# Performance work log

Measured on AMD Instinct MI355X. Metric: run time of the kernel, lower is better.

The kernel has to match this reference:

```python
import jax, jax.numpy as jnp
import numpy as np

# LIF neuron constants (standard mem_update)
THRESH = 0.5
LENS = 0.5
DECAY = 0.25
EPS = 1e-5
NUM_HEADS = 8

@jax.custom_vjp
def act_fun(mem):
    return (mem > THRESH).astype(mem.dtype)

def _act_fwd(mem):
    return act_fun(mem), mem

def _act_bwd(mem, g):
    surrogate = (jnp.abs(mem - THRESH) < LENS).astype(g.dtype)
    return (g * surrogate,)

act_fun.defvjp(_act_fwd, _act_bwd)

def mem_update(x):
    # x: (T, ...) -> binary spikes (T, ...) via recurrent LIF dynamics
    def step(carry, xt):
        mem_old, spike = carry
        # spike is detached in the reset gate (torch .detach())
        mem = mem_old * DECAY * (1.0 - jax.lax.stop_gradient(spike)) + xt
        s = act_fun(mem)
        return (mem, s), s
    init = (jnp.zeros_like(x[0]), jnp.zeros_like(x[0]))
    _, out = jax.lax.scan(step, init, x)
    return out

def bn(x, gamma, beta, mean, var):
    # inference-mode BatchNorm1d over channel dim of (T,B,C,L)
    inv = gamma / jnp.sqrt(var + EPS)
    return x * inv[None, None, :, None] + (beta - mean * inv)[None, None, :, None]

def setup_inputs() -> dict:
    key = jax.random.key(0)
    ks = jax.random.split(key, 11)
    T, B, C, L = 4, 2, 384, 1024
    s = 1.0 / np.sqrt(C)
    return {
        "x": jax.random.normal(ks[0], (T, B, C, L), jnp.float32),
        "W_w": jax.random.normal(ks[1], (2 * C, C), jnp.float32) * s,
        "bn1_gamma": jax.random.uniform(ks[2], (2 * C,), jnp.float32, 0.5, 1.5),
        "bn1_beta": jax.random.normal(ks[3], (2 * C,), jnp.float32) * 0.1,
        "bn1_mean": jax.random.normal(ks[4], (2 * C,), jnp.float32) * 0.1,
        "bn1_var": jax.random.uniform(ks[5], (2 * C,), jnp.float32, 0.5, 1.5),
        "proj_w": jax.random.normal(ks[6], (C, C), jnp.float32) * s,
        "bn2_gamma": jax.random.uniform(ks[7], (C,), jnp.float32, 0.5, 1.5),
        "bn2_beta": jax.random.normal(ks[8], (C,), jnp.float32) * 0.1,
        "bn2_mean": jax.random.normal(ks[9], (C,), jnp.float32) * 0.1,
        "bn2_var": jax.random.uniform(ks[10], (C,), jnp.float32, 0.5, 1.5),
    }

def reference(x, W_w, bn1_gamma, bn1_beta, bn1_mean, bn1_var, proj_w, bn2_gamma, bn2_beta, bn2_mean, bn2_var):
    T, B, C, L = x.shape
    H = NUM_HEADS
    d = C // H
    x_feat = x
    xs = mem_update(x)                                   # binary spikes (T,B,C,L)
    y = jnp.einsum('oc,tbcl->tbol', W_w, xs)             # 1x1 conv C->2C
    y = bn(y, bn1_gamma, bn1_beta, bn1_mean, bn1_var)
    y = y.reshape(T, B, H, 2 * d, L)
    y1, y2 = y[:, :, :, :d, :], y[:, :, :, d:, :]
    xr = xs.reshape(T, B, H, d, L)
    attn = jnp.einsum('tbhdl,tbhdm->tbhlm', y1, xr)      # (L,L) per head
    attn = mem_update(attn)                              # binary spikes
    out = jnp.einsum('tbhdl,tbhlm->tbhdm', y2, attn)
    out = out.reshape(T, B, C, L)
    out = mem_update(out)
    out = jnp.einsum('oc,tbcl->tbol', proj_w, out)       # Wproj 1x1
    out = bn(out, bn2_gamma, bn2_beta, bn2_mean, bn2_var)
    return out + x_feat
```

## Files before the change

kernel.cpp:

```cpp
#include <hip/hip_runtime.h>

#define T_  4
#define B_  2
#define C_  384
#define L_  1024
#define H_  8
#define C2_ 768
#define S_  (B_*C_*L_)

typedef __attribute__((ext_vector_type(8))) short short8;
typedef __attribute__((ext_vector_type(4))) float floatx4;
typedef __attribute__((ext_vector_type(16))) float floatx16;

__device__ __forceinline__ unsigned bf16_rne(float v) {
    unsigned u = __float_as_uint(v);
    u += 0x7FFFu + ((u >> 16) & 1u);
    return u >> 16;
}
__device__ __forceinline__ float bf16_to_f(unsigned h) { return __uint_as_float(h << 16); }
__device__ __forceinline__ void split3(float v, unsigned& hi, unsigned& mi, unsigned& lo) {
    hi = bf16_rne(v);
    float r1 = v - bf16_to_f(hi);
    mi = bf16_rne(r1);
    float r2 = r1 - bf16_to_f(mi);
    lo = bf16_rne(r2);
}

__global__ __launch_bounds__(256) void scan_and_split(
    const float* __restrict__ src, unsigned short* __restrict__ dstT,
    unsigned short* __restrict__ xsF,
    const float* __restrict__ Wa, int n4a,
    unsigned short* __restrict__ hia, unsigned short* __restrict__ mia,
    unsigned short* __restrict__ loa,
    const float* __restrict__ Wb, int n4b,
    unsigned short* __restrict__ hib, unsigned short* __restrict__ mib,
    unsigned short* __restrict__ lob) {
    __shared__ unsigned short tile[64][72];
    const int tid = threadIdx.x;
    if (blockIdx.x >= 192) {
        int i = (blockIdx.x - 192) * 256 + tid;
        const float* W; unsigned short *hi, *mi, *lo;
        if (i < n4a) { W = Wa; hi = hia; mi = mia; lo = loa; }
        else {
            i -= n4a;
            if (i >= n4b) return;
            W = Wb; hi = hib; mi = mib; lo = lob;
        }
        float4 v = ((const float4*)W)[i];
        float vv[4] = {v.x, v.y, v.z, v.w};
        union { unsigned short us[4]; uint2 u2; } h, m, l;
#pragma unroll
        for (int e = 0; e < 4; e++) {
            unsigned hh, mm, ll; split3(vv[e], hh, mm, ll);
            h.us[e] = (unsigned short)hh; m.us[e] = (unsigned short)mm; l.us[e] = (unsigned short)ll;
        }
        ((uint2*)hi)[i] = h.u2; ((uint2*)mi)[i] = m.u2; ((uint2*)lo)[i] = l.u2;
        return;
    }
    const int job = blockIdx.x;
    const int l0 = (job & 15) * 64;
    const int c0 = ((job >> 4) % 6) * 64;
    const int b  = job / 96;
    const int row = tid >> 2, seg = tid & 3;
    float mem[16], sp[16];
#pragma unroll
    for (int e = 0; e < 16; e++) { mem[e] = 0.f; sp[e] = 0.f; }
    for (int t = 0; t < T_; t++) {
        const size_t base = ((size_t)((t*B_ + b)*C_ + c0 + row))*L_ + l0 + seg*16;
#pragma unroll
        for (int qq = 0; qq < 4; qq++) {
            float4 v = *(const float4*)(src + base + qq*4);
            float vv[4] = {v.x, v.y, v.z, v.w};
            unsigned bs[4];
#pragma unroll
            for (int s = 0; s < 4; s++) {
                int e = qq*4 + s;
                mem[e] = mem[e]*0.25f*(1.f - sp[e]) + vv[s];
                bool sb = mem[e] > 0.5f;
                sp[e] = sb ? 1.f : 0.f;
                bs[s] = sb ? 0x3F80u : 0u;
            }
            *(unsigned*)&tile[row][seg*16 + qq*4]     = bs[0] | (bs[1] << 16);
            *(unsigned*)&tile[row][seg*16 + qq*4 + 2] = bs[2] | (bs[3] << 16);
        }
        __syncthreads();
        {
            const int lr = tid >> 2, cs = tid & 3;
#pragma unroll
            for (int sub = 0; sub < 2; sub++) {
                unsigned wv[4];
#pragma unroll
                for (int p = 0; p < 4; p++) {
                    unsigned e0 = tile[cs*16 + sub*8 + p*2][lr];
                    unsigned e1 = tile[cs*16 + sub*8 + p*2 + 1][lr];
                    wv[p] = e0 | (e1 << 16);
                }
                uint4 o; o.x = wv[0]; o.y = wv[1]; o.z = wv[2]; o.w = wv[3];
                const int cc = c0 + cs*16 + sub*8;
                *(uint4*)(dstT + ((size_t)(t*B_ + b)*L_ + l0 + lr)*C_ + cc) = o;
                const int hh = cc / 48, kc = (cc % 48) >> 3;
                *(uint4*)(xsF + ((((size_t)(t*B_ + b)*H_ + hh)*6 + kc)*L_ + l0 + lr)*8) = o;
            }
        }
        __syncthreads();
    }
}

__global__ __launch_bounds__(256) void scan_transpose(const float* __restrict__ src,
                                                      unsigned short* __restrict__ dstT) {
    __shared__ unsigned short tile[64][72];
    const int tid = threadIdx.x;
    const int l0 = blockIdx.x * 64, c0 = blockIdx.y * 64, b = blockIdx.z;
    const int row = tid >> 2, seg = tid & 3;
    float mem[16], sp[16];
#pragma unroll
    for (int e = 0; e < 16; e++) { mem[e] = 0.f; sp[e] = 0.f; }
    for (int t = 0; t < T_; t++) {
        const size_t base = ((size_t)((t*B_ + b)*C_ + c0 + row))*L_ + l0 + seg*16;
#pragma unroll
        for (int qq = 0; qq < 4; qq++) {
            float4 v = *(const float4*)(src + base + qq*4);
            float vv[4] = {v.x, v.y, v.z, v.w};
            unsigned bs[4];
#pragma unroll
            for (int s = 0; s < 4; s++) {
                int e = qq*4 + s;
                mem[e] = mem[e]*0.25f*(1.f - sp[e]) + vv[s];
                bool sb = mem[e] > 0.5f;
                sp[e] = sb ? 1.f : 0.f;
                bs[s] = sb ? 0x3F80u : 0u;
            }
            *(unsigned*)&tile[row][seg*16 + qq*4]     = bs[0] | (bs[1] << 16);
            *(unsigned*)&tile[row][seg*16 + qq*4 + 2] = bs[2] | (bs[3] << 16);
        }
        __syncthreads();
        {
            const int lr = tid >> 2, cs = tid & 3;
#pragma unroll
            for (int sub = 0; sub < 2; sub++) {
                unsigned wv[4];
#pragma unroll
                for (int p = 0; p < 4; p++) {
                    unsigned e0 = tile[cs*16 + sub*8 + p*2][lr];
                    unsigned e1 = tile[cs*16 + sub*8 + p*2 + 1][lr];
                    wv[p] = e0 | (e1 << 16);
                }
                uint4 o; o.x = wv[0]; o.y = wv[1]; o.z = wv[2]; o.w = wv[3];
                *(uint4*)(dstT + ((size_t)(t*B_ + b)*L_ + l0 + lr)*C_ + c0 + cs*16 + sub*8) = o;
            }
        }
        __syncthreads();
    }
}

__global__ __launch_bounds__(256) void gemm1_mfma(
    const unsigned short* __restrict__ whi, const unsigned short* __restrict__ wmi,
    const unsigned short* __restrict__ wlo, const unsigned short* __restrict__ xsT,
    const float* __restrict__ g, const float* __restrict__ be,
    const float* __restrict__ mn, const float* __restrict__ vr,
    unsigned short* __restrict__ y1hi, unsigned short* __restrict__ y1mi,
    unsigned short* __restrict__ y1lo,
    unsigned short* __restrict__ y2hi, unsigned short* __restrict__ y2mi,
    unsigned short* __restrict__ y2lo) {
    __shared__ unsigned short smem[14080];
    const int tid = threadIdx.x;
    const int flat = blockIdx.x;
    const int tb = flat & 7;
    const int ii = flat >> 3;
    const int mt = ii >> 4, lt = ii & 15;
    const int l0 = lt * 64;
    const int w = tid >> 6, lane = tid & 63;
    const int q = lane >> 4, n15 = lane & 15;
    const int mw = (w & 1) * 48, lw = (w >> 1) * 32;

    floatx4 acc[3][2];
#pragma unroll
    for (int i = 0; i < 3; i++)
#pragma unroll
        for (int j = 0; j < 2; j++) acc[i][j] = (floatx4){0.f,0.f,0.f,0.f};

    for (int ck = 0; ck < C_; ck += 32) {
#pragma unroll
        for (int p = 0; p < 3; p++) {
            const unsigned short* wp = p == 0 ? whi : p == 1 ? wmi : wlo;
            unsigned short* ap = smem + p*3840;
            for (int s = tid; s < 384; s += 256) {
                int r = s >> 2, c = s & 3;
                *(uint4*)&ap[r*40 + c*8] = *(const uint4*)(wp + (size_t)(mt*96 + r)*C_ + ck + c*8);
            }
        }
        {
            int r = tid >> 2, c = tid & 3;
            *(uint4*)&smem[11520 + r*40 + c*8] =
                *(const uint4*)(xsT + ((size_t)tb*L_ + l0 + r)*C_ + ck + c*8);
        }
        __syncthreads();
        short8 bb[2];
#pragma unroll
        for (int in = 0; in < 2; in++)
            bb[in] = *(short8*)&smem[11520 + (lw + in*16 + n15)*40 + q*8];
#pragma unroll
        for (int im = 0; im < 3; im++) {
            short8 ah = *(short8*)&smem[       (mw + im*16 + n15)*40 + q*8];
            short8 am = *(short8*)&smem[3840 + (mw + im*16 + n15)*40 + q*8];
            short8 al = *(short8*)&smem[7680 + (mw + im*16 + n15)*40 + q*8];
#pragma unroll
            for (int in = 0; in < 2; in++) {
                acc[im][in] = __builtin_amdgcn_mfma_f32_16x16x32_bf16(ah, bb[in], acc[im][in], 0,0,0);
                acc[im][in] = __builtin_amdgcn_mfma_f32_16x16x32_bf16(am, bb[in], acc[im][in], 0,0,0);
                acc[im][in] = __builtin_amdgcn_mfma_f32_16x16x32_bf16(al, bb[in], acc[im][in], 0,0,0);
            }
        }
        __syncthreads();
    }

#pragma unroll
    for (int im = 0; im < 3; im++)
#pragma unroll
        for (int r = 0; r < 4; r++) {
            int o = mt*96 + mw + im*16 + q*4 + r;
            float inv = g[o] / sqrtf(vr[o] + 1e-5f);
            float sh = be[o] - mn[o]*inv;
#pragma unroll
            for (int in = 0; in < 2; in++)
                acc[im][in][r] = acc[im][in][r]*inv + sh;
        }
    const bool isY1 = ((w & 1) == 0);
#pragma unroll
    for (int p = 0; p < 3; p++) {
        if (isY1) {
#pragma unroll
            for (int im = 0; im < 3; im++)
#pragma unroll
                for (int in = 0; in < 2; in++) {
                    union { unsigned short us[4]; uint2 u2; } pk;
#pragma unroll
                    for (int r = 0; r < 4; r++) {
                        unsigned hh = bf16_rne(acc[im][in][r]);
                        pk.us[r] = (unsigned short)hh;
                        acc[im][in][r] -= bf16_to_f(hh);
                    }
                    *(uint2*)&smem[(lw + in*16 + n15)*56 + im*16 + q*4] = pk.u2;
                }
        } else {
#pragma unroll
            for (int im = 0; im < 3; im++)
#pragma unroll
                for (int in = 0; in < 2; in++)
#pragma unroll
                    for (int r = 0; r < 4; r++) {
                        unsigned hh = bf16_rne(acc[im][in][r]);
                        smem[3584 + (im*16 + q*4 + r)*72 + lw + in*16 + n15] = (unsigned short)hh;
                        acc[im][in][r] -= bf16_to_f(hh);
                    }
        }
        __syncthreads();
        unsigned short* y1p = p == 0 ? y1hi : p == 1 ? y1mi : y1lo;
        unsigned short* y2p = p == 0 ? y2hi : p == 1 ? y2mi : y2lo;
        for (int s = tid; s < 384; s += 256) {
            int c8 = s >> 6, r1 = s & 63;
            *(uint4*)(y1p + ((((size_t)tb*H_ + mt)*6 + c8)*L_ + l0 + r1)*8) =
                *(uint4*)&smem[r1*56 + c8*8];
        }
        for (int s = tid; s < 384; s += 256) {
            int cr = s >> 3, lq = s & 7;
            *(uint4*)(y2p + ((size_t)tb*C_ + mt*48 + cr)*L_ + l0 + lq*8) =
                *(uint4*)&smem[3584 + cr*72 + lq*8];
        }
        __syncthreads();
    }
}

__global__ __launch_bounds__(256, 4) void attn_spike_mfma(
    const unsigned short* __restrict__ y1hi, const unsigned short* __restrict__ y1mi,
    const unsigned short* __restrict__ y1lo, const unsigned short* __restrict__ xsF,
    unsigned* __restrict__ bits) {
    const int tid = threadIdx.x;
    const int flat = blockIdx.x;
    const int xcd = flat & 7;
    const int ii = flat >> 3;
    const int bh = xcd*2 + (ii >> 7);
    const int rr = ii & 127;
    const int b = bh >> 3, h = bh & 7;
    const int lbase = (rr >> 3) * 64;
    const int mbase = (rr & 7) * 128;
    const int w = tid >> 6, lane = tid & 63;
    const int l31 = lane & 31, half = lane >> 5;
    const int mrow = mbase + w*32 + l31;

    float mem[2][16];
#pragma unroll
    for (int il = 0; il < 2; il++)
#pragma unroll
        for (int r = 0; r < 16; r++) mem[il][r] = 0.f;

    for (int t = 0; t < T_; t++) {
        const int tb = t*B_ + b;
        const size_t fb = ((size_t)tb*H_ + h)*6*L_*8;
        const unsigned short* ya_hi = y1hi + fb;
        const unsigned short* ya_mi = y1mi + fb;
        const unsigned short* ya_lo = y1lo + fb;
        const unsigned short* xf    = xsF  + fb;

        short8 bb[3];
#pragma unroll
        for (int ks = 0; ks < 3; ks++)
            bb[ks] = *(const short8*)(xf + ((size_t)(ks*2 + half)*L_ + mrow)*8);

        floatx16 acc[2];
#pragma unroll
        for (int il = 0; il < 2; il++)
#pragma unroll
            for (int r = 0; r < 16; r++) acc[il][r] = 0.f;

#pragma unroll
        for (int ks = 0; ks < 3; ks++) {
#pragma unroll
            for (int il = 0; il < 2; il++) {
                const size_t aoff = ((size_t)(ks*2 + half)*L_ + lbase + il*32 + l31)*8;
                short8 ah = *(const short8*)(ya_hi + aoff);
                short8 am = *(const short8*)(ya_mi + aoff);
                short8 al = *(const short8*)(ya_lo + aoff);
                acc[il] = __builtin_amdgcn_mfma_f32_32x32x16_bf16(ah, bb[ks], acc[il], 0,0,0);
                acc[il] = __builtin_amdgcn_mfma_f32_32x32x16_bf16(am, bb[ks], acc[il], 0,0,0);
                acc[il] = __builtin_amdgcn_mfma_f32_32x32x16_bf16(al, bb[ks], acc[il], 0,0,0);
            }
        }

        unsigned wds[2];
#pragma unroll
        for (int il = 0; il < 2; il++) {
            unsigned word = 0;
#pragma unroll
            for (int r = 0; r < 16; r++) {
                float m = (mem[il][r] > 0.5f ? 0.f : mem[il][r]*0.25f) + acc[il][r];
                mem[il][r] = m;
                int lloc = (r & 3) + 8*(r >> 2) + 4*half;
                word |= (m > 0.5f) ? (1u << lloc) : 0u;
            }
            wds[il] = word;
        }
        unsigned f0 = wds[0] | __shfl_xor(wds[0], 32);
        unsigned f1 = wds[1] | __shfl_xor(wds[1], 32);
        if (half == 0) {
            uint2 o; o.x = f0; o.y = f1;
            *(uint2*)(bits + ((size_t)(tb*H_ + h)*L_ + mrow)*32 + (lbase >> 5)) = o;
        }
    }
}

__global__ __launch_bounds__(256) void attn_out_mfma(
    const unsigned short* __restrict__ y2hi, const unsigned short* __restrict__ y2mi,
    const unsigned short* __restrict__ y2lo,
    const unsigned* __restrict__ bits, float* __restrict__ outpre) {
    __shared__ unsigned short A_hi[48][72], A_mi[48][72], A_lo[48][72];
    const int tid = threadIdx.x;
    const int flat = blockIdx.x;
    const int xcd = flat & 7;
    const int ii = flat >> 3;
    const int tbh = xcd*8 + (ii >> 3);
    const int mtile = ii & 7;
    const int t = tbh >> 4, b = (tbh >> 3) & 1, h = tbh & 7;
    const int tb = t*B_ + b;
    const int w = tid >> 6, lane = tid & 63;
    const int q = lane >> 4, n15 = lane & 15;
    const int mb = mtile*128 + w*32;

    floatx4 acc[3][2];
#pragma unroll
    for (int i = 0; i < 3; i++)
#pragma unroll
        for (int in = 0; in < 2; in++) acc[i][in] = (floatx4){0.f,0.f,0.f,0.f};

    const unsigned* brow0 = bits + ((size_t)(tb*H_ + h)*L_ + mb + n15)*32;
    const unsigned* brow1 = brow0 + 16*32;
    const size_t y2b = ((size_t)tb*C_ + h*48)*L_;

    for (int lt = 0; lt < L_; lt += 64) {
        for (int s = tid; s < 384; s += 256) {
            int r = s >> 3, c = s & 7;
            size_t ro = y2b + (size_t)r*L_ + lt + c*8;
            *(uint4*)&A_hi[r][c*8] = *(const uint4*)(y2hi + ro);
            *(uint4*)&A_mi[r][c*8] = *(const uint4*)(y2mi + ro);
            *(uint4*)&A_lo[r][c*8] = *(const uint4*)(y2lo + ro);
        }
        uint2 bw0 = *(const uint2*)(brow0 + (lt >> 5));
        uint2 bw1 = *(const uint2*)(brow1 + (lt >> 5));
        __syncthreads();
#pragma unroll
        for (int kc = 0; kc < 2; kc++) {
            unsigned word0 = kc ? bw0.y : bw0.x;
            unsigned word1 = kc ? bw1.y : bw1.x;
            unsigned byt0 = (word0 >> (q*8)) & 0xFFu;
            unsigned byt1 = (word1 >> (q*8)) & 0xFFu;
            union { unsigned u[4]; short8 v; } bu0, bu1;
#pragma unroll
            for (int p = 0; p < 4; p++) {
                bu0.u[p] = (((byt0 >> (2*p)) & 1u) ? 0x3F80u : 0u)
                         | (((byt0 >> (2*p+1)) & 1u) ? 0x3F800000u : 0u);
                bu1.u[p] = (((byt1 >> (2*p)) & 1u) ? 0x3F80u : 0u)
                         | (((byt1 >> (2*p+1)) & 1u) ? 0x3F800000u : 0u);
            }
            short8 bf0 = bu0.v, bf1 = bu1.v;
#pragma unroll
            for (int i = 0; i < 3; i++) {
                int ra = i*16 + n15;
                short8 ah = *(short8*)&A_hi[ra][kc*32 + q*8];
                short8 am = *(short8*)&A_mi[ra][kc*32 + q*8];
                short8 al = *(short8*)&A_lo[ra][kc*32 + q*8];
                acc[i][0] = __builtin_amdgcn_mfma_f32_16x16x32_bf16(ah, bf0, acc[i][0], 0,0,0);
                acc[i][0] = __builtin_amdgcn_mfma_f32_16x16x32_bf16(am, bf0, acc[i][0], 0,0,0);
                acc[i][0] = __builtin_amdgcn_mfma_f32_16x16x32_bf16(al, bf0, acc[i][0], 0,0,0);
                acc[i][1] = __builtin_amdgcn_mfma_f32_16x16x32_bf16(ah, bf1, acc[i][1], 0,0,0);
                acc[i][1] = __builtin_amdgcn_mfma_f32_16x16x32_bf16(am, bf1, acc[i][1], 0,0,0);
                acc[i][1] = __builtin_amdgcn_mfma_f32_16x16x32_bf16(al, bf1, acc[i][1], 0,0,0);
            }
        }
        __syncthreads();
    }
#pragma unroll
    for (int i = 0; i < 3; i++)
#pragma unroll
        for (int r = 0; r < 4; r++) {
            int d = i*16 + q*4 + r;
#pragma unroll
            for (int in = 0; in < 2; in++)
                outpre[((size_t)tb*C_ + h*48 + d)*L_ + mb + in*16 + n15] = acc[i][in][r];
        }
}

__global__ __launch_bounds__(256) void gemm2_mfma(
    const unsigned short* __restrict__ whi, const unsigned short* __restrict__ wmi,
    const unsigned short* __restrict__ wlo, const unsigned short* __restrict__ xT,
    const float* __restrict__ g, const float* __restrict__ be,
    const float* __restrict__ mn, const float* __restrict__ vr,
    const float* __restrict__ res, float* __restrict__ out) {
    __shared__ unsigned short A_hi[96][40], A_mi[96][40], A_lo[96][40];
    __shared__ unsigned short B_s[64][40];
    const int tid = threadIdx.x;
    const int tb = blockIdx.y;
    const int mt = blockIdx.x >> 4, lt = blockIdx.x & 15;
    const int l0 = lt * 64;
    const int w = tid >> 6, lane = tid & 63;
    const int q = lane >> 4, n15 = lane & 15;
    const int mw = (w & 1) * 48, lw = (w >> 1) * 32;

    floatx4 acc[3][2];
#pragma unroll
    for (int i = 0; i < 3; i++)
#pragma unroll
        for (int j = 0; j < 2; j++) acc[i][j] = (floatx4){0.f,0.f,0.f,0.f};

    for (int ck = 0; ck < C_; ck += 32) {
#pragma unroll
        for (int p = 0; p < 3; p++) {
            const unsigned short* wp = p == 0 ? whi : p == 1 ? wmi : wlo;
            unsigned short (*ap)[40] = p == 0 ? A_hi : p == 1 ? A_mi : A_lo;
            for (int s = tid; s < 384; s += 256) {
                int r = s >> 2, c = s & 3;
                *(uint4*)&ap[r][c*8] = *(const uint4*)(wp + (size_t)(mt*96 + r)*C_ + ck + c*8);
            }
        }
        {
            int r = tid >> 2, c4 = tid & 3;
            *(uint4*)&B_s[r][c4*8] = *(const uint4*)(xT + ((size_t)tb*L_ + l0 + r)*C_ + ck + c4*8);
        }
        __syncthreads();
        short8 bb[2];
#pragma unroll
        for (int in = 0; in < 2; in++)
            bb[in] = *(short8*)&B_s[lw + in*16 + n15][q*8];
#pragma unroll
        for (int im = 0; im < 3; im++) {
            short8 ah = *(short8*)&A_hi[mw + im*16 + n15][q*8];
            short8 am = *(short8*)&A_mi[mw + im*16 + n15][q*8];
            short8 al = *(short8*)&A_lo[mw + im*16 + n15][q*8];
#pragma unroll
            for (int in = 0; in < 2; in++) {
                acc[im][in] = __builtin_amdgcn_mfma_f32_16x16x32_bf16(ah, bb[in], acc[im][in], 0,0,0);
                acc[im][in] = __builtin_amdgcn_mfma_f32_16x16x32_bf16(am, bb[in], acc[im][in], 0,0,0);
                acc[im][in] = __builtin_amdgcn_mfma_f32_16x16x32_bf16(al, bb[in], acc[im][in], 0,0,0);
            }
        }
        __syncthreads();
    }
#pragma unroll
    for (int im = 0; im < 3; im++)
#pragma unroll
        for (int r = 0; r < 4; r++) {
            int o = mt*96 + mw + im*16 + q*4 + r;
            float inv = g[o] / sqrtf(vr[o] + 1e-5f);
            float sh = be[o] - mn[o]*inv;
#pragma unroll
            for (int in = 0; in < 2; in++) {
                int l = l0 + lw + in*16 + n15;
                size_t idx = ((size_t)tb*C_ + o)*L_ + l;
                out[idx] = acc[im][in][r]*inv + sh + res[idx];
            }
        }
}

extern "C" void kernel_launch(void* const* d_in, const int* in_sizes, int n_in,
                              void* d_out, int out_size, void* d_ws, size_t ws_size,
                              hipStream_t stream) {
    const float* x   = (const float*)d_in[0];
    const float* W_w = (const float*)d_in[1];
    const float* g1  = (const float*)d_in[2];
    const float* b1  = (const float*)d_in[3];
    const float* m1  = (const float*)d_in[4];
    const float* v1  = (const float*)d_in[5];
    const float* pw  = (const float*)d_in[6];
    const float* g2  = (const float*)d_in[7];
    const float* b2  = (const float*)d_in[8];
    const float* m2  = (const float*)d_in[9];
    const float* v2  = (const float*)d_in[10];

    float* ws = (float*)d_ws;
    unsigned short* xsT  = (unsigned short*)ws;
    unsigned short* y1hi = (unsigned short*)(ws + 1572864);
    unsigned short* y1mi = (unsigned short*)(ws + 3145728);
    unsigned short* y1lo = (unsigned short*)(ws + 4718592);
    unsigned short* y2hi = (unsigned short*)(ws + 6291456);
    unsigned short* y2mi = (unsigned short*)(ws + 7864320);
    unsigned short* y2lo = (unsigned short*)(ws + 9437184);
    unsigned*       bits = (unsigned*)(ws + 11010048);
    unsigned short* wspl[3]  = {(unsigned short*)(ws + 13107200),
                                (unsigned short*)(ws + 13254656),
                                (unsigned short*)(ws + 13402112)};
    unsigned short* pwspl[3] = {(unsigned short*)(ws + 13549568),
                                (unsigned short*)(ws + 13623296),
                                (unsigned short*)(ws + 13697024)};
    unsigned short* xsF  = (unsigned short*)(ws + 13770752);
    float*          outpre = (float*)(ws + 1572864);
    unsigned short* outsT  = (unsigned short*)(ws + 4718592);
    float* out = (float*)d_out;

    scan_and_split<<<dim3(624), 256, 0, stream>>>(x, xsT, xsF,
                                                  W_w, C2_*C_/4, wspl[0], wspl[1], wspl[2],
                                                  pw,  C_*C_/4, pwspl[0], pwspl[1], pwspl[2]);
    gemm1_mfma<<<dim3(1024), 256, 0, stream>>>(wspl[0], wspl[1], wspl[2], xsT,
                                               g1, b1, m1, v1,
                                               y1hi, y1mi, y1lo, y2hi, y2mi, y2lo);
    attn_spike_mfma<<<dim3(2048), 256, 0, stream>>>(y1hi, y1mi, y1lo, xsF, bits);
    attn_out_mfma<<<dim3(512), 256, 0, stream>>>(y2hi, y2mi, y2lo, bits, outpre);
    scan_transpose<<<dim3(16, 6, B_), 256, 0, stream>>>(outpre, outsT);
    gemm2_mfma<<<dim3(64, 8), 256, 0, stream>>>(pwspl[0], pwspl[1], pwspl[2], outsT,
                                                g2, b2, m2, v2, x, out);
}
```

Before: 225.8 us.

## Split attn_out reduction over L, halve scan tiles, prefetch loads, relayout spike bits

The attn_out kernel now splits the L reduction into two halves. This doubles the block count, and the two partial outputs go to separate buffers that the following scan kernel sums. Both scan kernels use 32-channel tiles, which doubles their grid, and they prefetch the next timestep's input into registers. The spike bit-mask layout is changed so each attn_out thread reads contiguous uint2 words. The y2 tile loads are software-pipelined through registers. In exchange, the partial outputs cost an extra fp32 buffer write and read, and the two halves are summed in a different order, which can change float rounding near the spike threshold.

```diff
diff --git a/kernel.cpp b/kernel.cpp
--- a/kernel.cpp
+++ b/kernel.cpp
@@ -6,7 +6,6 @@
 #define L_  1024
 #define H_  8
 #define C2_ 768
-#define S_  (B_*C_*L_)
 
 typedef __attribute__((ext_vector_type(8))) short short8;
 typedef __attribute__((ext_vector_type(4))) float floatx4;
@@ -35,10 +34,10 @@
     const float* __restrict__ Wb, int n4b,
     unsigned short* __restrict__ hib, unsigned short* __restrict__ mib,
     unsigned short* __restrict__ lob) {
-    __shared__ unsigned short tile[64][72];
+    __shared__ unsigned short tile[32][72];
     const int tid = threadIdx.x;
-    if (blockIdx.x >= 192) {
-        int i = (blockIdx.x - 192) * 256 + tid;
+    if (blockIdx.x >= 384) {
+        int i = (blockIdx.x - 384) * 256 + tid;
         const float* W; unsigned short *hi, *mi, *lo;
         if (i < n4a) { W = Wa; hi = hia; mi = mia; lo = loa; }
         else {
@@ -59,95 +58,106 @@
     }
     const int job = blockIdx.x;
     const int l0 = (job & 15) * 64;
-    const int c0 = ((job >> 4) % 6) * 64;
-    const int b  = job / 96;
-    const int row = tid >> 2, seg = tid & 3;
-    float mem[16], sp[16];
-#pragma unroll
-    for (int e = 0; e < 16; e++) { mem[e] = 0.f; sp[e] = 0.f; }
+    const int c0 = ((job >> 4) % 12) * 32;
+    const int b  = job / 192;
+    const int row = tid >> 3, seg = tid & 7;
+    float mem[8], sp[8];
+#pragma unroll
+    for (int e = 0; e < 8; e++) { mem[e] = 0.f; sp[e] = 0.f; }
+    const size_t base0 = ((size_t)(b*C_ + c0 + row))*L_ + l0 + seg*8;
+    float4 nx0 = *(const float4*)(src + base0);
+    float4 nx1 = *(const float4*)(src + base0 + 4);
     for (int t = 0; t < T_; t++) {
-        const size_t base = ((size_t)((t*B_ + b)*C_ + c0 + row))*L_ + l0 + seg*16;
-#pragma unroll
-        for (int qq = 0; qq < 4; qq++) {
-            float4 v = *(const float4*)(src + base + qq*4);
-            float vv[4] = {v.x, v.y, v.z, v.w};
-            unsigned bs[4];
-#pragma unroll
-            for (int s = 0; s < 4; s++) {
-                int e = qq*4 + s;
-                mem[e] = mem[e]*0.25f*(1.f - sp[e]) + vv[s];
-                bool sb = mem[e] > 0.5f;
-                sp[e] = sb ? 1.f : 0.f;
-                bs[s] = sb ? 0x3F80u : 0u;
-            }
-            *(unsigned*)&tile[row][seg*16 + qq*4]     = bs[0] | (bs[1] << 16);
-            *(unsigned*)&tile[row][seg*16 + qq*4 + 2] = bs[2] | (bs[3] << 16);
-        }
+        float4 v0 = nx0, v1 = nx1;
+        if (t < 3) {
+            const size_t nb = ((size_t)(((t+1)*B_ + b)*C_ + c0 + row))*L_ + l0 + seg*8;
+            nx0 = *(const float4*)(src + nb);
+            nx1 = *(const float4*)(src + nb + 4);
+        }
+        float vv[8] = {v0.x,v0.y,v0.z,v0.w,v1.x,v1.y,v1.z,v1.w};
+        unsigned bs[8];
+#pragma unroll
+        for (int e = 0; e < 8; e++) {
+            mem[e] = mem[e]*0.25f*(1.f - sp[e]) + vv[e];
+            bool sb = mem[e] > 0.5f;
+            sp[e] = sb ? 1.f : 0.f;
+            bs[e] = sb ? 0x3F80u : 0u;
+        }
+#pragma unroll
+        for (int p2 = 0; p2 < 4; p2++)
+            *(unsigned*)&tile[row][seg*8 + p2*2] = bs[p2*2] | (bs[p2*2+1] << 16);
         __syncthreads();
         {
             const int lr = tid >> 2, cs = tid & 3;
-#pragma unroll
-            for (int sub = 0; sub < 2; sub++) {
-                unsigned wv[4];
-#pragma unroll
-                for (int p = 0; p < 4; p++) {
-                    unsigned e0 = tile[cs*16 + sub*8 + p*2][lr];
-                    unsigned e1 = tile[cs*16 + sub*8 + p*2 + 1][lr];
-                    wv[p] = e0 | (e1 << 16);
-                }
-                uint4 o; o.x = wv[0]; o.y = wv[1]; o.z = wv[2]; o.w = wv[3];
-                const int cc = c0 + cs*16 + sub*8;
-                *(uint4*)(dstT + ((size_t)(t*B_ + b)*L_ + l0 + lr)*C_ + cc) = o;
-                const int hh = cc / 48, kc = (cc % 48) >> 3;
-                *(uint4*)(xsF + ((((size_t)(t*B_ + b)*H_ + hh)*6 + kc)*L_ + l0 + lr)*8) = o;
-            }
-        }
-        __syncthreads();
-    }
-}
-
-__global__ __launch_bounds__(256) void scan_transpose(const float* __restrict__ src,
-                                                      unsigned short* __restrict__ dstT) {
-    __shared__ unsigned short tile[64][72];
+            unsigned wv[4];
+#pragma unroll
+            for (int p = 0; p < 4; p++) {
+                unsigned e0 = tile[cs*8 + p*2][lr];
+                unsigned e1 = tile[cs*8 + p*2 + 1][lr];
+                wv[p] = e0 | (e1 << 16);
+            }
+            uint4 o; o.x = wv[0]; o.y = wv[1]; o.z = wv[2]; o.w = wv[3];
+            const int cc = c0 + cs*8;
+            *(uint4*)(dstT + ((size_t)(t*B_ + b)*L_ + l0 + lr)*C_ + cc) = o;
+            const int hh = cc / 48, kc = (cc % 48) >> 3;
+            *(uint4*)(xsF + ((((size_t)(t*B_ + b)*H_ + hh)*6 + kc)*L_ + l0 + lr)*8) = o;
+        }
+        __syncthreads();
+    }
+}
+
+__global__ __launch_bounds__(256) void scan_transpose2(
+    const float* __restrict__ srcA, const float* __restrict__ srcB,
+    unsigned short* __restrict__ dstT) {
+    __shared__ unsigned short tile[32][72];
     const int tid = threadIdx.x;
-    const int l0 = blockIdx.x * 64, c0 = blockIdx.y * 64, b = blockIdx.z;
-    const int row = tid >> 2, seg = tid & 3;
-    float mem[16], sp[16];
-#pragma unroll
-    for (int e = 0; e < 16; e++) { mem[e] = 0.f; sp[e] = 0.f; }
+    const int job = blockIdx.x;
+    const int l0 = (job & 15) * 64;
+    const int c0 = ((job >> 4) % 12) * 32;
+    const int b  = job / 192;
+    const int row = tid >> 3, seg = tid & 7;
+    float mem[8], sp[8];
+#pragma unroll
+    for (int e = 0; e < 8; e++) { mem[e] = 0.f; sp[e] = 0.f; }
+    const size_t base0 = ((size_t)(b*C_ + c0 + row))*L_ + l0 + seg*8;
+    float4 na0 = *(const float4*)(srcA + base0);
+    float4 na1 = *(const float4*)(srcA + base0 + 4);
+    float4 nb0 = *(const float4*)(srcB + base0);
+    float4 nb1 = *(const float4*)(srcB + base0 + 4);
     for (int t = 0; t < T_; t++) {
-        const size_t base = ((size_t)((t*B_ + b)*C_ + c0 + row))*L_ + l0 + seg*16;
-#pragma unroll
-        for (int qq = 0; qq < 4; qq++) {
-            float4 v = *(const float4*)(src + base + qq*4);
-            float vv[4] = {v.x, v.y, v.z, v.w};
-            unsigned bs[4];
-#pragma unroll
-            for (int s = 0; s < 4; s++) {
-                int e = qq*4 + s;
-                mem[e] = mem[e]*0.25f*(1.f - sp[e]) + vv[s];
-                bool sb = mem[e] > 0.5f;
-                sp[e] = sb ? 1.f : 0.f;
-                bs[s] = sb ? 0x3F80u : 0u;
-            }
-            *(unsigned*)&tile[row][seg*16 + qq*4]     = bs[0] | (bs[1] << 16);
-            *(unsigned*)&tile[row][seg*16 + qq*4 + 2] = bs[2] | (bs[3] << 16);
-        }
+        float4 a0 = na0, a1 = na1, b0 = nb0, b1 = nb1;
+        if (t < 3) {
+            const size_t nb = ((size_t)(((t+1)*B_ + b)*C_ + c0 + row))*L_ + l0 + seg*8;
+            na0 = *(const float4*)(srcA + nb);
+            na1 = *(const float4*)(srcA + nb + 4);
+            nb0 = *(const float4*)(srcB + nb);
+            nb1 = *(const float4*)(srcB + nb + 4);
+        }
+        float vv[8] = {a0.x+b0.x, a0.y+b0.y, a0.z+b0.z, a0.w+b0.w,
+                       a1.x+b1.x, a1.y+b1.y, a1.z+b1.z, a1.w+b1.w};
+        unsigned bs[8];
+#pragma unroll
+        for (int e = 0; e < 8; e++) {
+            mem[e] = mem[e]*0.25f*(1.f - sp[e]) + vv[e];
+            bool sb = mem[e] > 0.5f;
+            sp[e] = sb ? 1.f : 0.f;
+            bs[e] = sb ? 0x3F80u : 0u;
+        }
+#pragma unroll
+        for (int p2 = 0; p2 < 4; p2++)
+            *(unsigned*)&tile[row][seg*8 + p2*2] = bs[p2*2] | (bs[p2*2+1] << 16);
         __syncthreads();
         {
             const int lr = tid >> 2, cs = tid & 3;
-#pragma unroll
-            for (int sub = 0; sub < 2; sub++) {
-                unsigned wv[4];
-#pragma unroll
-                for (int p = 0; p < 4; p++) {
-                    unsigned e0 = tile[cs*16 + sub*8 + p*2][lr];
-                    unsigned e1 = tile[cs*16 + sub*8 + p*2 + 1][lr];
-                    wv[p] = e0 | (e1 << 16);
-                }
-                uint4 o; o.x = wv[0]; o.y = wv[1]; o.z = wv[2]; o.w = wv[3];
-                *(uint4*)(dstT + ((size_t)(t*B_ + b)*L_ + l0 + lr)*C_ + c0 + cs*16 + sub*8) = o;
-            }
+            unsigned wv[4];
+#pragma unroll
+            for (int p = 0; p < 4; p++) {
+                unsigned e0 = tile[cs*8 + p*2][lr];
+                unsigned e1 = tile[cs*8 + p*2 + 1][lr];
+                wv[p] = e0 | (e1 << 16);
+            }
+            uint4 o; o.x = wv[0]; o.y = wv[1]; o.z = wv[2]; o.w = wv[3];
+            *(uint4*)(dstT + ((size_t)(t*B_ + b)*L_ + l0 + lr)*C_ + c0 + cs*8) = o;
         }
         __syncthreads();
     }
@@ -344,7 +354,7 @@
         unsigned f1 = wds[1] | __shfl_xor(wds[1], 32);
         if (half == 0) {
             uint2 o; o.x = f0; o.y = f1;
-            *(uint2*)(bits + ((size_t)(tb*H_ + h)*L_ + mrow)*32 + (lbase >> 5)) = o;
+            ((uint2*)bits)[((size_t)(tb*H_ + h)*16 + (lbase >> 6))*1024 + mrow] = o;
         }
     }
 }
@@ -352,19 +362,22 @@
 __global__ __launch_bounds__(256) void attn_out_mfma(
     const unsigned short* __restrict__ y2hi, const unsigned short* __restrict__ y2mi,
     const unsigned short* __restrict__ y2lo,
-    const unsigned* __restrict__ bits, float* __restrict__ outpre) {
+    const unsigned* __restrict__ bits,
+    float* __restrict__ outpre, float* __restrict__ outpre2) {
     __shared__ unsigned short A_hi[48][72], A_mi[48][72], A_lo[48][72];
     const int tid = threadIdx.x;
     const int flat = blockIdx.x;
     const int xcd = flat & 7;
     const int ii = flat >> 3;
-    const int tbh = xcd*8 + (ii >> 3);
-    const int mtile = ii & 7;
+    const int tbh = xcd*8 + (ii >> 4);
+    const int mtile = (ii >> 1) & 7;
+    const int ls = ii & 1;
     const int t = tbh >> 4, b = (tbh >> 3) & 1, h = tbh & 7;
     const int tb = t*B_ + b;
     const int w = tid >> 6, lane = tid & 63;
     const int q = lane >> 4, n15 = lane & 15;
     const int mb = mtile*128 + w*32;
+    const int lt0 = ls * 512;
 
     floatx4 acc[3][2];
 #pragma unroll
@@ -372,21 +385,39 @@
 #pragma unroll
         for (int in = 0; in < 2; in++) acc[i][in] = (floatx4){0.f,0.f,0.f,0.f};
 
-    const unsigned* brow0 = bits + ((size_t)(tb*H_ + h)*L_ + mb + n15)*32;
-    const unsigned* brow1 = brow0 + 16*32;
+    const uint2* bvec = (const uint2*)bits;
+    const size_t bbase = ((size_t)(tb*H_ + h)*16)*1024 + mb + n15;
     const size_t y2b = ((size_t)tb*C_ + h*48)*L_;
 
-    for (int lt = 0; lt < L_; lt += 64) {
-        for (int s = tid; s < 384; s += 256) {
-            int r = s >> 3, c = s & 7;
-            size_t ro = y2b + (size_t)r*L_ + lt + c*8;
-            *(uint4*)&A_hi[r][c*8] = *(const uint4*)(y2hi + ro);
-            *(uint4*)&A_mi[r][c*8] = *(const uint4*)(y2mi + ro);
-            *(uint4*)&A_lo[r][c*8] = *(const uint4*)(y2lo + ro);
-        }
-        uint2 bw0 = *(const uint2*)(brow0 + (lt >> 5));
-        uint2 bw1 = *(const uint2*)(brow1 + (lt >> 5));
-        __syncthreads();
+    const int r0 = tid >> 3, c0i = tid & 7;
+    const int r1 = (tid + 256) >> 3, c1i = tid & 7;
+    uint4 rh0, rm0, rl0, rh1, rm1, rl1;
+    {
+        size_t ro = y2b + (size_t)r0*L_ + lt0 + c0i*8;
+        rh0 = *(const uint4*)(y2hi + ro); rm0 = *(const uint4*)(y2mi + ro); rl0 = *(const uint4*)(y2lo + ro);
+        if (tid < 128) {
+            size_t ro1 = y2b + (size_t)r1*L_ + lt0 + c1i*8;
+            rh1 = *(const uint4*)(y2hi + ro1); rm1 = *(const uint4*)(y2mi + ro1); rl1 = *(const uint4*)(y2lo + ro1);
+        }
+    }
+
+    for (int it = 0; it < 8; it++) {
+        const int lt = lt0 + it*64;
+        *(uint4*)&A_hi[r0][c0i*8] = rh0; *(uint4*)&A_mi[r0][c0i*8] = rm0; *(uint4*)&A_lo[r0][c0i*8] = rl0;
+        if (tid < 128) {
+            *(uint4*)&A_hi[r1][c1i*8] = rh1; *(uint4*)&A_mi[r1][c1i*8] = rm1; *(uint4*)&A_lo[r1][c1i*8] = rl1;
+        }
+        uint2 bw0 = bvec[bbase + (size_t)(lt >> 6)*1024];
+        uint2 bw1 = bvec[bbase + (size_t)(lt >> 6)*1024 + 16];
+        __syncthreads();
+        if (it < 7) {
+            size_t ro = y2b + (size_t)r0*L_ + (lt + 64) + c0i*8;
+            rh0 = *(const uint4*)(y2hi + ro); rm0 = *(const uint4*)(y2mi + ro); rl0 = *(const uint4*)(y2lo + ro);
+            if (tid < 128) {
+                size_t ro1 = y2b + (size_t)r1*L_ + (lt + 64) + c1i*8;
+                rh1 = *(const uint4*)(y2hi + ro1); rm1 = *(const uint4*)(y2mi + ro1); rl1 = *(const uint4*)(y2lo + ro1);
+            }
+        }
 #pragma unroll
         for (int kc = 0; kc < 2; kc++) {
             unsigned word0 = kc ? bw0.y : bw0.x;
@@ -418,6 +449,7 @@
         }
         __syncthreads();
     }
+    float* outP = ls ? outpre2 : outpre;
 #pragma unroll
     for (int i = 0; i < 3; i++)
 #pragma unroll
@@ -425,7 +457,7 @@
             int d = i*16 + q*4 + r;
 #pragma unroll
             for (int in = 0; in < 2; in++)
-                outpre[((size_t)tb*C_ + h*48 + d)*L_ + mb + in*16 + n15] = acc[i][in][r];
+                outP[((size_t)tb*C_ + h*48 + d)*L_ + mb + in*16 + n15] = acc[i][in][r];
         }
 }
 
@@ -531,19 +563,20 @@
                                 (unsigned short*)(ws + 13623296),
                                 (unsigned short*)(ws + 13697024)};
     unsigned short* xsF  = (unsigned short*)(ws + 13770752);
-    float*          outpre = (float*)(ws + 1572864);
-    unsigned short* outsT  = (unsigned short*)(ws + 4718592);
+    float*          outpre  = (float*)(ws + 1572864);
+    float*          outpre2 = (float*)(ws + 14557184);
+    unsigned short* outsT   = (unsigned short*)(ws + 4718592);
     float* out = (float*)d_out;
 
-    scan_and_split<<<dim3(624), 256, 0, stream>>>(x, xsT, xsF,
+    scan_and_split<<<dim3(816), 256, 0, stream>>>(x, xsT, xsF,
                                                   W_w, C2_*C_/4, wspl[0], wspl[1], wspl[2],
                                                   pw,  C_*C_/4, pwspl[0], pwspl[1], pwspl[2]);
     gemm1_mfma<<<dim3(1024), 256, 0, stream>>>(wspl[0], wspl[1], wspl[2], xsT,
                                                g1, b1, m1, v1,
                                                y1hi, y1mi, y1lo, y2hi, y2mi, y2lo);
     attn_spike_mfma<<<dim3(2048), 256, 0, stream>>>(y1hi, y1mi, y1lo, xsF, bits);
-    attn_out_mfma<<<dim3(512), 256, 0, stream>>>(y2hi, y2mi, y2lo, bits, outpre);
-    scan_transpose<<<dim3(16, 6, B_), 256, 0, stream>>>(outpre, outsT);
+    attn_out_mfma<<<dim3(1024), 256, 0, stream>>>(y2hi, y2mi, y2lo, bits, outpre, outpre2);
+    scan_transpose2<<<dim3(384), 256, 0, stream>>>(outpre, outpre2, outsT);
     gemm2_mfma<<<dim3(64, 8), 256, 0, stream>>>(pwspl[0], pwspl[1], pwspl[2], outsT,
                                                 g2, b2, m2, v2, x, out);
 }
```

Result: faster. 212.3 us (-6.0%).
